# Performance work log

Measured on AMD Instinct MI355X. Metric: run time of the kernel, lower is better.

Reference implementation:

```python
import jax, jax.numpy as jnp
import numpy as np
import math

B, S, H, NH = 2, 2048, 1024, 16
DH = H // NH  # 64
REL_VOCAB = 4096  # 2 * (max_position_embeddings // 4)


def setup_inputs() -> dict:
    key = jax.random.key(0)
    ks = jax.random.split(key, 9)
    s = 0.02
    return {
        "hidden_states": jax.random.normal(ks[0], (B, S, H), jnp.float32),
        "attention_mask": jnp.zeros((B, 1, 1, S), jnp.float32),
        "distance_idx": jax.random.randint(ks[1], (S, S), 0, REL_VOCAB),
        "Wq": jax.random.normal(ks[2], (H, H), jnp.float32) * s,
        "bq": jnp.zeros((H,), jnp.float32),
        "Wk": jax.random.normal(ks[3], (H, H), jnp.float32) * s,
        "bk": jnp.zeros((H,), jnp.float32),
        "Wv": jax.random.normal(ks[4], (H, H), jnp.float32) * s,
        "bv": jnp.zeros((H,), jnp.float32),
        "dist_emb": jax.random.normal(ks[5], (REL_VOCAB, NH), jnp.float32) * s,
    }


def _heads(x):
    # [B,S,H] -> [B,NH,S,DH]
    return x.reshape(B, S, NH, DH).transpose(0, 2, 1, 3)


def reference(hidden_states, attention_mask, distance_idx, Wq, bq, Wk, bk, Wv, bv, dist_emb):
    q = _heads(hidden_states @ Wq.T + bq)
    k = _heads(hidden_states @ Wk.T + bk)
    v = _heads(hidden_states @ Wv.T + bv)
    # scores: [B,NH,S,S]
    scores = jnp.einsum("bhqd,bhkd->bhqk", q, k) / math.sqrt(DH)
    # relative_scalar_bias: embed(distance_idx) [S,S,NH] -> [1,NH,S,S]
    bias = dist_emb[distance_idx].transpose(2, 0, 1)[None]
    scores = scores + bias  # attention_scores_terms == 1 -> /sqrt(1)
    scores = scores + attention_mask
    probs = jax.nn.softmax(scores, axis=-1)
    ctx = jnp.einsum("bhqk,bhkd->bhqd", probs, v)
    return ctx.transpose(0, 2, 1, 3).reshape(B, S, H)
```

## Files before the change

kernel.cpp:

```cpp
#include <hip/hip_runtime.h>
#include <hip/hip_bf16.h>

#define B_   2
#define S_   2048
#define H_   1024
#define NH_  16
#define DH_  64

typedef __attribute__((ext_vector_type(8))) __bf16 bf16x8;
typedef __attribute__((ext_vector_type(8))) unsigned short u16x8;
typedef __attribute__((ext_vector_type(4))) float f32x4;

typedef const __attribute__((address_space(1))) unsigned int gu32_t;
typedef __attribute__((address_space(3))) unsigned int su32_t;

static __device__ inline unsigned short f2bf(float x) {
    union { float f; unsigned u; } v; v.f = x;
    unsigned r = v.u + 0x7fffu + ((v.u >> 16) & 1u);
    return (unsigned short)(r >> 16);
}

static __device__ inline unsigned short f2bf_r(float x) {
    union { float f; unsigned u; } v; v.f = x;
    return (unsigned short)((v.u + 0x8000u) >> 16);
}

static __device__ inline float bf2f(unsigned short u) {
    union { unsigned u; float f; } v; v.u = ((unsigned)u) << 16;
    return v.f;
}

static __device__ inline bf16x8 ldfrag(const unsigned short* p) {
    return __builtin_bit_cast(bf16x8, *(const u16x8*)p);
}

__global__ void conv_all(const float* __restrict__ x,
                         const float* __restrict__ Wq, const float* __restrict__ Wk,
                         const float* __restrict__ Wv, const float* __restrict__ demb,
                         unsigned short* __restrict__ xb, unsigned short* __restrict__ wall,
                         unsigned short* __restrict__ dembT) {
    int bid = blockIdx.x, tid = threadIdx.x;
    if (bid < 4096) {
        int i = bid * 256 + tid;
        float4 v = ((const float4*)x)[i];
        ushort4 o;
        o.x = f2bf(v.x); o.y = f2bf(v.y); o.z = f2bf(v.z); o.w = f2bf(v.w);
        ((ushort4*)xb)[i] = o;
    } else if (bid < 7168) {
        int i = (bid - 4096) * 256 + tid;
        int e = i * 4;
        int which = e >> 20;
        int r4 = (e & ((1 << 20) - 1)) >> 2;
        const float* src = which == 0 ? Wq : which == 1 ? Wk : Wv;
        float4 v = ((const float4*)src)[r4];
        ushort4 o;
        o.x = f2bf(v.x); o.y = f2bf(v.y); o.z = f2bf(v.z); o.w = f2bf(v.w);
        ((ushort4*)wall)[i] = o;
    } else {
        int t = (bid - 7168) * 256 + tid;
        int h = t >> 12, e = t & 4095;
        dembT[t] = f2bf(demb[e * 16 + h]);
    }
}

__global__ __launch_bounds__(256) void gemm_qkv(
    const unsigned short* __restrict__ Xb, const unsigned short* __restrict__ Wall,
    const float* __restrict__ bq, const float* __restrict__ bk, const float* __restrict__ bv,
    unsigned short* __restrict__ Q, unsigned short* __restrict__ K, unsigned short* __restrict__ V)
{
    __shared__ unsigned short As[128 * 32];
    __shared__ unsigned short Bs[128 * 32];
    const int tid = threadIdx.x, lane = tid & 63, wv = tid >> 6;
    const int g = lane >> 4, l16 = lane & 15;
    const int wm = wv >> 1, wn = wv & 1;
    const int bm = blockIdx.y, bn = blockIdx.x;

    const int lrow = lane >> 2, lcol = (lane & 3) * 8;

    f32x4 acc[4][4];
    #pragma unroll
    for (int i = 0; i < 4; ++i)
        #pragma unroll
        for (int j = 0; j < 4; ++j) acc[i][j] = (f32x4){0.f, 0.f, 0.f, 0.f};

    for (int kt = 0; kt < 32; ++kt) {
        #pragma unroll
        for (int i = 0; i < 2; ++i) {
            int chunk = wv * 2 + i;
            int row = chunk * 16 + lrow;
            const unsigned short* ga = &Xb[(size_t)(bm * 128 + row) * 1024 + kt * 32 + lcol];
            const unsigned short* gb = &Wall[(size_t)(bn * 128 + row) * 1024 + kt * 32 + lcol];
            __builtin_amdgcn_global_load_lds((gu32_t*)(const void*)ga, (su32_t*)(void*)&As[chunk * 512], 16, 0, 0);
            __builtin_amdgcn_global_load_lds((gu32_t*)(const void*)gb, (su32_t*)(void*)&Bs[chunk * 512], 16, 0, 0);
        }
        __syncthreads();
        bf16x8 a[4], b[4];
        #pragma unroll
        for (int mi = 0; mi < 4; ++mi) a[mi] = ldfrag(&As[(wm * 64 + mi * 16 + l16) * 32 + g * 8]);
        #pragma unroll
        for (int ni = 0; ni < 4; ++ni) b[ni] = ldfrag(&Bs[(wn * 64 + ni * 16 + l16) * 32 + g * 8]);
        #pragma unroll
        for (int mi = 0; mi < 4; ++mi)
            #pragma unroll
            for (int ni = 0; ni < 4; ++ni)
                acc[mi][ni] = __builtin_amdgcn_mfma_f32_16x16x32_bf16(a[mi], b[ni], acc[mi][ni], 0, 0, 0);
        __syncthreads();
    }

    #pragma unroll
    for (int mi = 0; mi < 4; ++mi) {
        #pragma unroll
        for (int ni = 0; ni < 4; ++ni) {
            int gn = bn * 128 + wn * 64 + ni * 16 + l16;
            int which = gn >> 10, nn = gn & 1023;
            int h = nn >> 6, d = nn & 63;
            float bias = which == 0 ? bq[nn] : which == 1 ? bk[nn] : bv[nn];
            unsigned short* dst = which == 0 ? Q : which == 1 ? K : V;
            #pragma unroll
            for (int r = 0; r < 4; ++r) {
                int gm = bm * 128 + wm * 64 + mi * 16 + g * 4 + r;
                int bb = gm >> 11, s = gm & 2047;
                dst[((size_t)(bb * 16 + h) * 2048 + s) * 64 + d] = f2bf(acc[mi][ni][r] + bias);
            }
        }
    }
}

__global__ void transpose_v(const unsigned short* __restrict__ V, unsigned short* __restrict__ VT) {
    __shared__ unsigned short t[64][65];
    int bh = blockIdx.y, st = blockIdx.x, tid = threadIdx.x;
    size_t ib = (size_t)bh * S_ * DH_ + (size_t)st * 64 * 64;
    #pragma unroll
    for (int rep = 0; rep < 16; ++rep) {
        int e = rep * 256 + tid;
        t[e >> 6][e & 63] = V[ib + e];
    }
    __syncthreads();
    size_t ob = (size_t)bh * DH_ * S_ + st * 64;
    #pragma unroll
    for (int rep = 0; rep < 16; ++rep) {
        int e = rep * 256 + tid;
        int d = e >> 6, sl = e & 63;
        VT[ob + (size_t)d * S_ + sl] = t[sl][d];
    }
}

__global__ __launch_bounds__(256, 4) void attn(
    const unsigned short* __restrict__ Q, const unsigned short* __restrict__ K,
    const unsigned short* __restrict__ VT, const int* __restrict__ didx,
    const unsigned short* __restrict__ dembT, const float* __restrict__ mask,
    float* __restrict__ out)
{
    __shared__ unsigned short demb_h[4096];
    __shared__ unsigned short Ks[64 * 64];
    __shared__ unsigned short Vs[64 * 64];
    __shared__ unsigned short Ps[4][16 * 64];
    const int tid = threadIdx.x, lane = tid & 63, w = tid >> 6;
    const int g = lane >> 4, l16 = lane & 15;
    const int h = blockIdx.x, qt = blockIdx.y, b = blockIdx.z;
    const int bh = b * NH_ + h;
    const int qr = qt * 64 + w * 16;

    #pragma unroll
    for (int j = 0; j < 2; ++j) {
        int i = j * 256 + tid;
        *(uint4*)&demb_h[i * 8] = *(const uint4*)&dembT[h * 4096 + i * 8];
    }

    bf16x8 qf[2];
    {
        size_t qbase = ((size_t)bh * S_ + qr + l16) * DH_;
        qf[0] = ldfrag(&Q[qbase + g * 8]);
        qf[1] = ldfrag(&Q[qbase + 32 + g * 8]);
    }

    f32x4 oa[4];
    float lsum[4];
    #pragma unroll
    for (int i = 0; i < 4; ++i) {
        oa[i] = (f32x4){0.f, 0.f, 0.f, 0.f};
        lsum[i] = 0.f;
    }

    const size_t kbase = (size_t)bh * S_ * DH_;
    const size_t vbase = (size_t)bh * DH_ * S_;

    __syncthreads();

    for (int kt = 0; kt < 32; ++kt) {
        #pragma unroll
        for (int j = 0; j < 2; ++j) {
            int e = j * 2048 + tid * 8;
            int r = e >> 6, c = e & 63;
            int sidx = r * 64 + ((((c >> 3) ^ (r & 7))) << 3);
            *(uint4*)&Ks[sidx] = *(const uint4*)&K[kbase + (size_t)kt * 64 * 64 + e];
            *(uint4*)&Vs[sidx] = *(const uint4*)&VT[vbase + (size_t)r * S_ + kt * 64 + c];
        }

        int ei[4][4];
        float mk[4];
        #pragma unroll
        for (int kj = 0; kj < 4; ++kj) {
            int kg = kt * 64 + kj * 16 + l16;
            mk[kj] = mask[b * S_ + kg];
            #pragma unroll
            for (int r = 0; r < 4; ++r) {
                int qg = qr + g * 4 + r;
                ei[kj][r] = didx[qg * S_ + kg];
            }
        }

        __syncthreads();

        f32x4 sc[4];
        #pragma unroll
        for (int kj = 0; kj < 4; ++kj) {
            int row = kj * 16 + l16, m = row & 7;
            bf16x8 kf0 = ldfrag(&Ks[row * 64 + ((g ^ m) << 3)]);
            bf16x8 kf1 = ldfrag(&Ks[row * 64 + (((g + 4) ^ m) << 3)]);
            f32x4 z = (f32x4){0.f, 0.f, 0.f, 0.f};
            z = __builtin_amdgcn_mfma_f32_16x16x32_bf16(qf[0], kf0, z, 0, 0, 0);
            z = __builtin_amdgcn_mfma_f32_16x16x32_bf16(qf[1], kf1, z, 0, 0, 0);
            sc[kj] = z;
        }

        #pragma unroll
        for (int kj = 0; kj < 4; ++kj) {
            #pragma unroll
            for (int r = 0; r < 4; ++r) {
                float bm = bf2f(demb_h[ei[kj][r]]) + mk[kj];
                float p = __expf(fmaf(sc[kj][r], 0.125f, bm));
                lsum[r] += p;
                int row = g * 4 + r;
                int idx = row * 64 + ((((kj * 2 + (l16 >> 3)) ^ (row & 7))) << 3) + (l16 & 7);
                Ps[w][idx] = f2bf_r(p);
            }
        }

        int pm = l16 & 7;
        bf16x8 pf0 = ldfrag(&Ps[w][l16 * 64 + ((g ^ pm) << 3)]);
        bf16x8 pf1 = ldfrag(&Ps[w][l16 * 64 + (((g + 4) ^ pm) << 3)]);
        #pragma unroll
        for (int dt = 0; dt < 4; ++dt) {
            int row = dt * 16 + l16, m = row & 7;
            bf16x8 vf0 = ldfrag(&Vs[row * 64 + ((g ^ m) << 3)]);
            bf16x8 vf1 = ldfrag(&Vs[row * 64 + (((g + 4) ^ m) << 3)]);
            oa[dt] = __builtin_amdgcn_mfma_f32_16x16x32_bf16(pf0, vf0, oa[dt], 0, 0, 0);
            oa[dt] = __builtin_amdgcn_mfma_f32_16x16x32_bf16(pf1, vf1, oa[dt], 0, 0, 0);
        }
        __syncthreads();
    }

    float linv[4];
    #pragma unroll
    for (int r = 0; r < 4; ++r) {
        float s = lsum[r];
        s += __shfl_xor(s, 1);
        s += __shfl_xor(s, 2);
        s += __shfl_xor(s, 4);
        s += __shfl_xor(s, 8);
        linv[r] = __builtin_amdgcn_rcpf(s);
    }

    #pragma unroll
    for (int dt = 0; dt < 4; ++dt) {
        #pragma unroll
        for (int r = 0; r < 4; ++r) {
            int s = qr + g * 4 + r;
            int d = dt * 16 + l16;
            out[((size_t)b * S_ + s) * H_ + h * DH_ + d] = oa[dt][r] * linv[r];
        }
    }
}

extern "C" void kernel_launch(void* const* d_in, const int* in_sizes, int n_in,
                              void* d_out, int out_size, void* d_ws, size_t ws_size,
                              hipStream_t stream) {
    const float* hidden = (const float*)d_in[0];
    const float* mask   = (const float*)d_in[1];
    const int*   didx   = (const int*)d_in[2];
    const float* Wq     = (const float*)d_in[3];
    const float* bq     = (const float*)d_in[4];
    const float* Wk     = (const float*)d_in[5];
    const float* bk     = (const float*)d_in[6];
    const float* Wv     = (const float*)d_in[7];
    const float* bv     = (const float*)d_in[8];
    const float* demb   = (const float*)d_in[9];
    float* out = (float*)d_out;

    unsigned short* ws = (unsigned short*)d_ws;
    unsigned short* Xb   = ws;
    unsigned short* Wall = Xb + 4096 * 1024;
    unsigned short* Qb   = Wall + 3072 * 1024;
    unsigned short* Kb   = Qb + 4194304;
    unsigned short* Vb   = Kb + 4194304;
    unsigned short* VTb  = Vb + 4194304;
    unsigned short* DembT = VTb + 4194304;

    conv_all<<<7424, 256, 0, stream>>>(hidden, Wq, Wk, Wv, demb, Xb, Wall, DembT);
    gemm_qkv<<<dim3(24, 32), 256, 0, stream>>>(Xb, Wall, bq, bk, bv, Qb, Kb, Vb);
    transpose_v<<<dim3(32, 32), 256, 0, stream>>>(Vb, VTb);
    attn<<<dim3(16, 32, 2), 256, 0, stream>>>(Qb, Kb, VTb, didx, DembT, mask, out);
}
```

Before: 219.9 us.

## Prefetch next K/V tile and bias indices into registers; remap grid for locality

The attention kernel now loads the next iteration's K/V tiles, mask values and distance indices into registers while the current tile is computed. It double-buffers the index arrays with a two-step unrolled loop, which hides global-load latency behind the MFMA work. The launch also becomes a 1D grid whose block index is remapped so that groups of eight query tiles sharing a distance_idx region run across heads together, aiming at better L2 reuse. The cost is higher register pressure, which may reduce occupancy under the 4-blocks launch bound.

```diff
diff --git a/kernel.cpp b/kernel.cpp
--- a/kernel.cpp
+++ b/kernel.cpp
@@ -157,7 +157,10 @@
     __shared__ unsigned short Ps[4][16 * 64];
     const int tid = threadIdx.x, lane = tid & 63, w = tid >> 6;
     const int g = lane >> 4, l16 = lane & 15;
-    const int h = blockIdx.x, qt = blockIdx.y, b = blockIdx.z;
+    const int L = blockIdx.x;
+    const int h = (L >> 3) & 15;
+    const int qtb = ((L >> 7) << 3) + (L & 7);
+    const int qt = qtb & 31, b = qtb >> 5;
     const int bh = b * NH_ + h;
     const int qr = qt * 64 + w * 16;
 
@@ -185,28 +188,49 @@
     const size_t kbase = (size_t)bh * S_ * DH_;
     const size_t vbase = (size_t)bh * DH_ * S_;
 
+    const int e0 = tid * 8, e1 = 2048 + tid * 8;
+    const int r0 = e0 >> 6, c0 = e0 & 63;
+    const int r1 = e1 >> 6, c1 = e1 & 63;
+    const int s0 = r0 * 64 + ((((c0 >> 3) ^ (r0 & 7))) << 3);
+    const int s1 = r1 * 64 + ((((c1 >> 3) ^ (r1 & 7))) << 3);
+
+    uint4 kr0, kr1, vr0, vr1;
+    int eiA[4][4], eiB[4][4];
+    float mkA[4], mkB[4];
+
+    kr0 = *(const uint4*)&K[kbase + e0];
+    kr1 = *(const uint4*)&K[kbase + e1];
+    vr0 = *(const uint4*)&VT[vbase + (size_t)r0 * S_ + c0];
+    vr1 = *(const uint4*)&VT[vbase + (size_t)r1 * S_ + c1];
+    #pragma unroll
+    for (int kj = 0; kj < 4; ++kj) {
+        int kg = kj * 16 + l16;
+        mkA[kj] = mask[b * S_ + kg];
+        #pragma unroll
+        for (int r = 0; r < 4; ++r)
+            eiA[kj][r] = didx[(qr + g * 4 + r) * S_ + kg];
+    }
+
     __syncthreads();
 
-    for (int kt = 0; kt < 32; ++kt) {
-        #pragma unroll
-        for (int j = 0; j < 2; ++j) {
-            int e = j * 2048 + tid * 8;
-            int r = e >> 6, c = e & 63;
-            int sidx = r * 64 + ((((c >> 3) ^ (r & 7))) << 3);
-            *(uint4*)&Ks[sidx] = *(const uint4*)&K[kbase + (size_t)kt * 64 * 64 + e];
-            *(uint4*)&Vs[sidx] = *(const uint4*)&VT[vbase + (size_t)r * S_ + kt * 64 + c];
-        }
-
-        int ei[4][4];
-        float mk[4];
-        #pragma unroll
-        for (int kj = 0; kj < 4; ++kj) {
-            int kg = kt * 64 + kj * 16 + l16;
-            mk[kj] = mask[b * S_ + kg];
+    auto body = [&](int kt, int (&ei)[4][4], float (&mk)[4], int (&ein)[4][4], float (&mkn)[4]) {
+        if (kt) __syncthreads();
+        *(uint4*)&Ks[s0] = kr0; *(uint4*)&Ks[s1] = kr1;
+        *(uint4*)&Vs[s0] = vr0; *(uint4*)&Vs[s1] = vr1;
+
+        if (kt < 31) {
+            int kn = kt + 1;
+            kr0 = *(const uint4*)&K[kbase + (size_t)kn * 4096 + e0];
+            kr1 = *(const uint4*)&K[kbase + (size_t)kn * 4096 + e1];
+            vr0 = *(const uint4*)&VT[vbase + (size_t)r0 * S_ + kn * 64 + c0];
+            vr1 = *(const uint4*)&VT[vbase + (size_t)r1 * S_ + kn * 64 + c1];
             #pragma unroll
-            for (int r = 0; r < 4; ++r) {
-                int qg = qr + g * 4 + r;
-                ei[kj][r] = didx[qg * S_ + kg];
+            for (int kj = 0; kj < 4; ++kj) {
+                int kg = kn * 64 + kj * 16 + l16;
+                mkn[kj] = mask[b * S_ + kg];
+                #pragma unroll
+                for (int r = 0; r < 4; ++r)
+                    ein[kj][r] = didx[(qr + g * 4 + r) * S_ + kg];
             }
         }
 
@@ -248,7 +272,11 @@
             oa[dt] = __builtin_amdgcn_mfma_f32_16x16x32_bf16(pf0, vf0, oa[dt], 0, 0, 0);
             oa[dt] = __builtin_amdgcn_mfma_f32_16x16x32_bf16(pf1, vf1, oa[dt], 0, 0, 0);
         }
-        __syncthreads();
+    };
+
+    for (int k2 = 0; k2 < 16; ++k2) {
+        body(2 * k2,     eiA, mkA, eiB, mkB);
+        body(2 * k2 + 1, eiB, mkB, eiA, mkA);
     }
 
     float linv[4];
@@ -300,5 +328,5 @@
     conv_all<<<7424, 256, 0, stream>>>(hidden, Wq, Wk, Wv, demb, Xb, Wall, DembT);
     gemm_qkv<<<dim3(24, 32), 256, 0, stream>>>(Xb, Wall, bq, bk, bv, Qb, Kb, Vb);
     transpose_v<<<dim3(32, 32), 256, 0, stream>>>(Vb, VTb);
-    attn<<<dim3(16, 32, 2), 256, 0, stream>>>(Qb, Kb, VTb, didx, DembT, mask, out);
-}
+    attn<<<1024, 256, 0, stream>>>(Qb, Kb, VTb, didx, DembT, mask, out);
+}
```

After: 399.2 us. +81.5%, slower.

## Double-buffer QKV GEMM tiles, register-prefetch K/V in attention, use exp2

Applied to the files above, without the earlier changes.

The QKV projection GEMM now double-buffers its LDS tiles, issuing the next k-tile's global-to-LDS loads before computing the current one and dropping one barrier per iteration. The attention kernel prefetches the next K/V tile into registers while the current tile is computed, and moves the trailing barrier to the top of the loop. It also folds log2(e) into the bias table, mask and score scale so it can use the native exp2 instead of expf. The aim is to hide global-memory latency in both kernels, at the cost of more LDS and registers, which may lower occupancy.

```diff
diff --git a/kernel.cpp b/kernel.cpp
--- a/kernel.cpp
+++ b/kernel.cpp
@@ -6,6 +6,8 @@
 #define H_   1024
 #define NH_  16
 #define DH_  64
+
+#define LOG2E 1.44269504f
 
 typedef __attribute__((ext_vector_type(8))) __bf16 bf16x8;
 typedef __attribute__((ext_vector_type(8))) unsigned short u16x8;
@@ -59,7 +61,7 @@
     } else {
         int t = (bid - 7168) * 256 + tid;
         int h = t >> 12, e = t & 4095;
-        dembT[t] = f2bf(demb[e * 16 + h]);
+        dembT[t] = f2bf(demb[e * 16 + h] * LOG2E);
     }
 }
 
@@ -68,8 +70,8 @@
     const float* __restrict__ bq, const float* __restrict__ bk, const float* __restrict__ bv,
     unsigned short* __restrict__ Q, unsigned short* __restrict__ K, unsigned short* __restrict__ V)
 {
-    __shared__ unsigned short As[128 * 32];
-    __shared__ unsigned short Bs[128 * 32];
+    __shared__ unsigned short As[2][128 * 32];
+    __shared__ unsigned short Bs[2][128 * 32];
     const int tid = threadIdx.x, lane = tid & 63, wv = tid >> 6;
     const int g = lane >> 4, l16 = lane & 15;
     const int wm = wv >> 1, wn = wv & 1;
@@ -83,28 +85,40 @@
         #pragma unroll
         for (int j = 0; j < 4; ++j) acc[i][j] = (f32x4){0.f, 0.f, 0.f, 0.f};
 
+    #pragma unroll
+    for (int i = 0; i < 2; ++i) {
+        int chunk = wv * 2 + i;
+        int row = chunk * 16 + lrow;
+        const unsigned short* ga = &Xb[(size_t)(bm * 128 + row) * 1024 + lcol];
+        const unsigned short* gb = &Wall[(size_t)(bn * 128 + row) * 1024 + lcol];
+        __builtin_amdgcn_global_load_lds((gu32_t*)(const void*)ga, (su32_t*)(void*)&As[0][chunk * 512], 16, 0, 0);
+        __builtin_amdgcn_global_load_lds((gu32_t*)(const void*)gb, (su32_t*)(void*)&Bs[0][chunk * 512], 16, 0, 0);
+    }
+
     for (int kt = 0; kt < 32; ++kt) {
-        #pragma unroll
-        for (int i = 0; i < 2; ++i) {
-            int chunk = wv * 2 + i;
-            int row = chunk * 16 + lrow;
-            const unsigned short* ga = &Xb[(size_t)(bm * 128 + row) * 1024 + kt * 32 + lcol];
-            const unsigned short* gb = &Wall[(size_t)(bn * 128 + row) * 1024 + kt * 32 + lcol];
-            __builtin_amdgcn_global_load_lds((gu32_t*)(const void*)ga, (su32_t*)(void*)&As[chunk * 512], 16, 0, 0);
-            __builtin_amdgcn_global_load_lds((gu32_t*)(const void*)gb, (su32_t*)(void*)&Bs[chunk * 512], 16, 0, 0);
-        }
+        const int cur = kt & 1;
         __syncthreads();
+        if (kt < 31) {
+            #pragma unroll
+            for (int i = 0; i < 2; ++i) {
+                int chunk = wv * 2 + i;
+                int row = chunk * 16 + lrow;
+                const unsigned short* ga = &Xb[(size_t)(bm * 128 + row) * 1024 + (kt + 1) * 32 + lcol];
+                const unsigned short* gb = &Wall[(size_t)(bn * 128 + row) * 1024 + (kt + 1) * 32 + lcol];
+                __builtin_amdgcn_global_load_lds((gu32_t*)(const void*)ga, (su32_t*)(void*)&As[cur ^ 1][chunk * 512], 16, 0, 0);
+                __builtin_amdgcn_global_load_lds((gu32_t*)(const void*)gb, (su32_t*)(void*)&Bs[cur ^ 1][chunk * 512], 16, 0, 0);
+            }
+        }
         bf16x8 a[4], b[4];
         #pragma unroll
-        for (int mi = 0; mi < 4; ++mi) a[mi] = ldfrag(&As[(wm * 64 + mi * 16 + l16) * 32 + g * 8]);
-        #pragma unroll
-        for (int ni = 0; ni < 4; ++ni) b[ni] = ldfrag(&Bs[(wn * 64 + ni * 16 + l16) * 32 + g * 8]);
+        for (int mi = 0; mi < 4; ++mi) a[mi] = ldfrag(&As[cur][(wm * 64 + mi * 16 + l16) * 32 + g * 8]);
+        #pragma unroll
+        for (int ni = 0; ni < 4; ++ni) b[ni] = ldfrag(&Bs[cur][(wn * 64 + ni * 16 + l16) * 32 + g * 8]);
         #pragma unroll
         for (int mi = 0; mi < 4; ++mi)
             #pragma unroll
             for (int ni = 0; ni < 4; ++ni)
                 acc[mi][ni] = __builtin_amdgcn_mfma_f32_16x16x32_bf16(a[mi], b[ni], acc[mi][ni], 0, 0, 0);
-        __syncthreads();
     }
 
     #pragma unroll
@@ -185,16 +199,31 @@
     const size_t kbase = (size_t)bh * S_ * DH_;
     const size_t vbase = (size_t)bh * DH_ * S_;
 
+    const int e0 = tid * 8, e1 = 2048 + tid * 8;
+    const int r0 = e0 >> 6, c0 = e0 & 63;
+    const int r1 = e1 >> 6, c1 = e1 & 63;
+    const int s0 = r0 * 64 + ((((c0 >> 3) ^ (r0 & 7))) << 3);
+    const int s1 = r1 * 64 + ((((c1 >> 3) ^ (r1 & 7))) << 3);
+    const int dbase = (qr + g * 4) * S_ + l16;
+
+    uint4 kr0 = *(const uint4*)&K[kbase + e0];
+    uint4 kr1 = *(const uint4*)&K[kbase + e1];
+    uint4 vr0 = *(const uint4*)&VT[vbase + (size_t)r0 * S_ + c0];
+    uint4 vr1 = *(const uint4*)&VT[vbase + (size_t)r1 * S_ + c1];
+
     __syncthreads();
 
     for (int kt = 0; kt < 32; ++kt) {
-        #pragma unroll
-        for (int j = 0; j < 2; ++j) {
-            int e = j * 2048 + tid * 8;
-            int r = e >> 6, c = e & 63;
-            int sidx = r * 64 + ((((c >> 3) ^ (r & 7))) << 3);
-            *(uint4*)&Ks[sidx] = *(const uint4*)&K[kbase + (size_t)kt * 64 * 64 + e];
-            *(uint4*)&Vs[sidx] = *(const uint4*)&VT[vbase + (size_t)r * S_ + kt * 64 + c];
+        if (kt) __syncthreads();
+        *(uint4*)&Ks[s0] = kr0; *(uint4*)&Ks[s1] = kr1;
+        *(uint4*)&Vs[s0] = vr0; *(uint4*)&Vs[s1] = vr1;
+
+        if (kt < 31) {
+            int kn = kt + 1;
+            kr0 = *(const uint4*)&K[kbase + (size_t)kn * 4096 + e0];
+            kr1 = *(const uint4*)&K[kbase + (size_t)kn * 4096 + e1];
+            vr0 = *(const uint4*)&VT[vbase + (size_t)r0 * S_ + kn * 64 + c0];
+            vr1 = *(const uint4*)&VT[vbase + (size_t)r1 * S_ + kn * 64 + c1];
         }
 
         int ei[4][4];
@@ -202,12 +231,10 @@
         #pragma unroll
         for (int kj = 0; kj < 4; ++kj) {
             int kg = kt * 64 + kj * 16 + l16;
-            mk[kj] = mask[b * S_ + kg];
-            #pragma unroll
-            for (int r = 0; r < 4; ++r) {
-                int qg = qr + g * 4 + r;
-                ei[kj][r] = didx[qg * S_ + kg];
-            }
+            mk[kj] = mask[b * S_ + kg] * LOG2E;
+            #pragma unroll
+            for (int r = 0; r < 4; ++r)
+                ei[kj][r] = didx[dbase + r * S_ + kt * 64 + kj * 16];
         }
 
         __syncthreads();
@@ -229,7 +256,7 @@
             #pragma unroll
             for (int r = 0; r < 4; ++r) {
                 float bm = bf2f(demb_h[ei[kj][r]]) + mk[kj];
-                float p = __expf(fmaf(sc[kj][r], 0.125f, bm));
+                float p = __builtin_amdgcn_exp2f(fmaf(sc[kj][r], 0.125f * LOG2E, bm));
                 lsum[r] += p;
                 int row = g * 4 + r;
                 int idx = row * 64 + ((((kj * 2 + (l16 >> 3)) ^ (row & 7))) << 3) + (l16 & 7);
@@ -248,7 +275,6 @@
             oa[dt] = __builtin_amdgcn_mfma_f32_16x16x32_bf16(pf0, vf0, oa[dt], 0, 0, 0);
             oa[dt] = __builtin_amdgcn_mfma_f32_16x16x32_bf16(pf1, vf1, oa[dt], 0, 0, 0);
         }
-        __syncthreads();
     }
 
     float linv[4];
```

Measured after the change: 226.8 us. 3.1% more time.
